# Performance work log

Measured on AMD Instinct MI355X. Metric: run time of the kernel, lower is better.

The kernel has to match this reference:

```python
import jax, jax.numpy as jnp
import numpy as np
import math

D = 512  # feature dim (must equal Lv for the final bmm)

def setup_inputs() -> dict:
    key = jax.random.key(0)
    k1, k2, k3 = jax.random.split(key, 3)
    B, Lp, Lq, Lv = 32, 1024, 1024, 512
    linear_pre = jax.random.normal(k1, (B, Lp, D), dtype=jnp.float32)
    linear_q = jax.random.normal(k2, (B, Lq, D), dtype=jnp.float32)
    linear_v = jax.random.normal(k3, (B, Lv, D), dtype=jnp.float32)
    return {"linear_pre": linear_pre, "linear_q": linear_q, "linear_v": linear_v}

def reference(linear_pre, linear_q, linear_v):
    scale = 1.0 / math.sqrt(D)
    # Two parallel softmax-attention streams (exp / sum == softmax over last dim).
    # attnp: [B, Lp, Lq], attne: [B, Lq, Lv]
    attnp = jax.nn.softmax(jnp.einsum('bpd,bqd->bpq', linear_pre, linear_q) * scale, axis=-1)
    attne = jax.nn.softmax(jnp.einsum('bqd,bvd->bqv', linear_q, linear_v) * scale, axis=-1)
    # dropout is identity in eval mode (deterministic reference)
    precompute = jnp.einsum('bpq,bqd->bpd', attnp, linear_q)   # [B, Lp, D]
    energy = jnp.einsum('bqv,bvd->bqd', attne, linear_v)       # [B, Lq, D]
    # final bmm requires D == Lv
    weightedContext = jnp.einsum('bqv,bvd->bqd', energy, linear_v)  # [B, Lq, D]
    return (weightedContext, energy, precompute)
```

## Files before the change

kernel.cpp:

```cpp
#include <hip/hip_runtime.h>

#define BATCH 32
#define LP 1024
#define LQ 1024
#define LV 512
#define DIM 512

typedef __bf16 bf16x8 __attribute__((ext_vector_type(8)));
typedef float f32x4 __attribute__((ext_vector_type(4)));
typedef unsigned short ushort_t;
typedef unsigned short us8 __attribute__((ext_vector_type(8)));

__device__ __forceinline__ ushort_t f2bf(float f) {
  unsigned int u = __float_as_uint(f);
  unsigned int r = (u + 0x7FFFu + ((u >> 16) & 1u)) >> 16;
  return (ushort_t)r;
}

__device__ __forceinline__ void async16(const void* g, void* l) {
  __builtin_amdgcn_global_load_lds(
      (const __attribute__((address_space(1))) unsigned int*)g,
      (__attribute__((address_space(3))) unsigned int*)l, 16, 0, 0);
}

__global__ __launch_bounds__(256)
void cvt_kernel(const float* __restrict__ in, ushort_t* __restrict__ out) {
  int i = blockIdx.x * blockDim.x + threadIdx.x;
  const float4* p = (const float4*)in;
  float4 a = p[i * 2], b = p[i * 2 + 1];
  us8 h;
  h[0] = f2bf(a.x); h[1] = f2bf(a.y); h[2] = f2bf(a.z); h[3] = f2bf(a.w);
  h[4] = f2bf(b.x); h[5] = f2bf(b.y); h[6] = f2bf(b.z); h[7] = f2bf(b.w);
  *(us8*)&out[(size_t)i * 8] = h;
}

__global__ void transpose_cvt(const float* __restrict__ in, ushort_t* __restrict__ outT,
                              ushort_t* __restrict__ outR, int R, int C) {
  __shared__ ushort_t tile[32][33];
  int b = blockIdx.z;
  int c0 = blockIdx.x * 32, r0 = blockIdx.y * 32;
  const float* inb = in + (size_t)b * R * C;
  ushort_t* outTb = outT + (size_t)b * R * C;
  ushort_t* outRb = outR + (size_t)b * R * C;
  int x = threadIdx.x, y = threadIdx.y;
#pragma unroll
  for (int k = 0; k < 4; ++k) {
    int r = r0 + y + k * 8;
    ushort_t h = f2bf(inb[(size_t)r * C + c0 + x]);
    tile[y + k * 8][x] = h;
    outRb[(size_t)r * C + c0 + x] = h;
  }
  __syncthreads();
#pragma unroll
  for (int k = 0; k < 4; ++k) {
    int c = c0 + y + k * 8;
    outTb[(size_t)c * R + r0 + x] = tile[x][y + k * 8];
  }
}

__global__ __launch_bounds__(256)
void score_bf16_kernel(const ushort_t* __restrict__ A, const ushort_t* __restrict__ BT,
                       ushort_t* __restrict__ P, float* __restrict__ lsum,
                       int M, int N, int K) {
  __shared__ ushort_t sA[128 * 32];
  __shared__ ushort_t sB[128 * 32];
  int b = blockIdx.z;
  int m0 = blockIdx.x * 128, n0 = blockIdx.y * 128;
  const ushort_t* Ab = A + ((size_t)b * M + m0) * K;
  const ushort_t* Bb = BT + ((size_t)b * N + n0) * K;
  int tid = threadIdx.x;
  int lane = tid & 63, w = tid >> 6;
  int wm = w >> 1, wn = w & 1;
  int quad = lane >> 4, low = lane & 15;

  f32x4 acc[4][4];
  f32x4 zero = {0.f, 0.f, 0.f, 0.f};
#pragma unroll
  for (int i = 0; i < 4; ++i)
#pragma unroll
    for (int j = 0; j < 4; ++j) acc[i][j] = zero;

  for (int kt = 0; kt < K; kt += 32) {
#pragma unroll
    for (int j = 0; j < 2; ++j) {
      int cb = w * 128 + j * 64;
      int c = cb + lane;
      int r = c >> 2, kc = c & 3;
      async16(Ab + (size_t)r * K + kt + kc * 8, &sA[cb * 8]);
      async16(Bb + (size_t)r * K + kt + kc * 8, &sB[cb * 8]);
    }
    __syncthreads();
    bf16x8 af[4], bfr[4];
#pragma unroll
    for (int t = 0; t < 4; ++t) {
      af[t]  = *(const bf16x8*)&sA[(wm * 64 + t * 16 + low) * 32 + quad * 8];
      bfr[t] = *(const bf16x8*)&sB[(wn * 64 + t * 16 + low) * 32 + quad * 8];
    }
#pragma unroll
    for (int i = 0; i < 4; ++i)
#pragma unroll
      for (int j = 0; j < 4; ++j)
        acc[i][j] = __builtin_amdgcn_mfma_f32_16x16x32_bf16(af[i], bfr[j], acc[i][j], 0, 0, 0);
    __syncthreads();
  }

  const float sc = 0.04419417382415922f;
  size_t pb = (size_t)b * M * N;
#pragma unroll
  for (int i = 0; i < 4; ++i) {
    int gr0 = m0 + wm * 64 + i * 16 + quad * 4;
#pragma unroll
    for (int r = 0; r < 4; ++r) {
      int gr = gr0 + r;
      float rs = 0.f;
#pragma unroll
      for (int j = 0; j < 4; ++j) {
        float p = __expf(acc[i][j][r] * sc);
        rs += p;
        int gc = n0 + wn * 64 + j * 16 + low;
        P[pb + (size_t)gr * N + gc] = f2bf(p);
      }
      rs += __shfl_xor(rs, 1);
      rs += __shfl_xor(rs, 2);
      rs += __shfl_xor(rs, 4);
      rs += __shfl_xor(rs, 8);
      if (low == 0) atomicAdd(&lsum[(size_t)b * M + gr], rs);
    }
  }
}

template <bool DIV, bool OUT2>
__global__ __launch_bounds__(256)
void gemm_bt_kernel(const ushort_t* __restrict__ A, const ushort_t* __restrict__ BT,
                    const float* __restrict__ lsum, float* __restrict__ out,
                    ushort_t* __restrict__ out2, int M, int N, int K) {
  __shared__ ushort_t sA[128 * 32];
  __shared__ ushort_t sB[128 * 32];
  int b = blockIdx.z;
  int m0 = blockIdx.x * 128, n0 = blockIdx.y * 128;
  const ushort_t* Ab = A + ((size_t)b * M + m0) * K;
  const ushort_t* Bb = BT + ((size_t)b * N + n0) * K;
  int tid = threadIdx.x;
  int lane = tid & 63, w = tid >> 6;
  int wm = w >> 1, wn = w & 1;
  int quad = lane >> 4, low = lane & 15;

  f32x4 acc[4][4];
  f32x4 zero = {0.f, 0.f, 0.f, 0.f};
#pragma unroll
  for (int i = 0; i < 4; ++i)
#pragma unroll
    for (int j = 0; j < 4; ++j) acc[i][j] = zero;

  for (int kt = 0; kt < K; kt += 32) {
#pragma unroll
    for (int j = 0; j < 2; ++j) {
      int cb = w * 128 + j * 64;
      int c = cb + lane;
      int r = c >> 2, kc = c & 3;
      async16(Ab + (size_t)r * K + kt + kc * 8, &sA[cb * 8]);
      async16(Bb + (size_t)r * K + kt + kc * 8, &sB[cb * 8]);
    }
    __syncthreads();
    bf16x8 af[4], bfr[4];
#pragma unroll
    for (int t = 0; t < 4; ++t) {
      af[t]  = *(const bf16x8*)&sA[(wm * 64 + t * 16 + low) * 32 + quad * 8];
      bfr[t] = *(const bf16x8*)&sB[(wn * 64 + t * 16 + low) * 32 + quad * 8];
    }
#pragma unroll
    for (int i = 0; i < 4; ++i)
#pragma unroll
      for (int j = 0; j < 4; ++j)
        acc[i][j] = __builtin_amdgcn_mfma_f32_16x16x32_bf16(af[i], bfr[j], acc[i][j], 0, 0, 0);
    __syncthreads();
  }

  size_t ob = (size_t)b * M * N;
#pragma unroll
  for (int i = 0; i < 4; ++i) {
    int gr0 = m0 + wm * 64 + i * 16 + quad * 4;
#pragma unroll
    for (int r = 0; r < 4; ++r) {
      int gr = gr0 + r;
      float inv = 1.f;
      if (DIV) inv = 1.f / lsum[(size_t)b * M + gr];
#pragma unroll
      for (int j = 0; j < 4; ++j) {
        int gc = n0 + wn * 64 + j * 16 + low;
        float o = acc[i][j][r] * inv;
        out[ob + (size_t)gr * N + gc] = o;
        if (OUT2) out2[ob + (size_t)gr * N + gc] = f2bf(o);
      }
    }
  }
}

extern "C" void kernel_launch(void* const* d_in, const int* in_sizes, int n_in,
                              void* d_out, int out_size, void* d_ws, size_t ws_size,
                              hipStream_t stream) {
  (void)in_sizes; (void)n_in; (void)out_size; (void)ws_size;
  const float* pre = (const float*)d_in[0];
  const float* q   = (const float*)d_in[1];
  const float* v   = (const float*)d_in[2];

  float* out      = (float*)d_out;
  float* wc       = out;
  float* energy   = out + (size_t)BATCH * LQ * DIM;
  float* precomp  = out + 2 * (size_t)BATCH * LQ * DIM;

  char* ws = (char*)d_ws;
  size_t off = 0;
  auto alloc = [&](size_t bytes) {
    void* p = ws + off;
    off += (bytes + 255) & ~(size_t)255;
    return p;
  };
  ushort_t* preB = (ushort_t*)alloc((size_t)BATCH * LP * DIM * 2);
  ushort_t* qB   = (ushort_t*)alloc((size_t)BATCH * LQ * DIM * 2);
  ushort_t* vB   = (ushort_t*)alloc((size_t)BATCH * LV * DIM * 2);
  ushort_t* qT   = (ushort_t*)alloc((size_t)BATCH * DIM * LQ * 2);
  ushort_t* vT   = (ushort_t*)alloc((size_t)BATCH * DIM * LV * 2);
  ushort_t* Pp   = (ushort_t*)alloc((size_t)BATCH * LP * LQ * 2);
  ushort_t* Pe   = (ushort_t*)alloc((size_t)BATCH * LQ * LV * 2);
  ushort_t* Ebf  = (ushort_t*)alloc((size_t)BATCH * LQ * DIM * 2);
  float* lp = (float*)alloc((size_t)BATCH * LP * 4);
  float* le = (float*)alloc((size_t)BATCH * LQ * 4);

  hipMemsetAsync(lp, 0, (size_t)BATCH * (LP + LQ) * 4, stream);

  cvt_kernel<<<(size_t)BATCH * LP * DIM / 8 / 256, 256, 0, stream>>>(pre, preB);
  transpose_cvt<<<dim3(DIM / 32, LQ / 32, BATCH), dim3(32, 8), 0, stream>>>(q, qT, qB, LQ, DIM);
  transpose_cvt<<<dim3(DIM / 32, LV / 32, BATCH), dim3(32, 8), 0, stream>>>(v, vT, vB, LV, DIM);

  score_bf16_kernel<<<dim3(LP / 128, LQ / 128, BATCH), 256, 0, stream>>>(
      preB, qB, Pp, lp, LP, LQ, DIM);
  score_bf16_kernel<<<dim3(LQ / 128, LV / 128, BATCH), 256, 0, stream>>>(
      qB, vB, Pe, le, LQ, LV, DIM);

  gemm_bt_kernel<true, false><<<dim3(LP / 128, DIM / 128, BATCH), 256, 0, stream>>>(
      Pp, qT, lp, precomp, nullptr, LP, DIM, LQ);
  gemm_bt_kernel<true, true><<<dim3(LQ / 128, DIM / 128, BATCH), 256, 0, stream>>>(
      Pe, vT, le, energy, Ebf, LQ, DIM, LV);
  gemm_bt_kernel<false, false><<<dim3(LQ / 128, DIM / 128, BATCH), 256, 0, stream>>>(
      Ebf, vT, nullptr, wc, nullptr, LQ, DIM, LV);
}
```

Measured before the change: 598.8 us.

## Replace GEMMs with 256x256-tile double-buffered pipelined MFMA kernel

Merges the score and output GEMM kernels into one templated 256x256-tile kernel with 512 threads and 128KB of dynamic LDS. It double-buffers K tiles of 64 with async global-to-LDS loads, explicit vmcnt waits and raw barriers, XOR-swizzles the LDS columns to avoid bank conflicts, and raises wave priority around the MFMA blocks. The goal is more data reuse per tile and hiding global load latency behind matrix math. The cost is higher register and LDS pressure, fewer blocks (4x fewer tiles, e.g. 256 for the Pe score GEMM), and fragile hand-written synchronisation.

```diff
diff --git a/kernel.cpp b/kernel.cpp
--- a/kernel.cpp
+++ b/kernel.cpp
@@ -22,6 +22,9 @@
       (const __attribute__((address_space(1))) unsigned int*)g,
       (__attribute__((address_space(3))) unsigned int*)l, 16, 0, 0);
 }
+
+#define BARRIER() asm volatile("s_barrier" ::: "memory")
+#define VMCNT(n) asm volatile("s_waitcnt vmcnt(" #n ")" ::: "memory")
 
 __global__ __launch_bounds__(256)
 void cvt_kernel(const float* __restrict__ in, ushort_t* __restrict__ out) {
@@ -58,143 +61,163 @@
   }
 }
 
-__global__ __launch_bounds__(256)
-void score_bf16_kernel(const ushort_t* __restrict__ A, const ushort_t* __restrict__ BT,
-                       ushort_t* __restrict__ P, float* __restrict__ lsum,
-                       int M, int N, int K) {
-  __shared__ ushort_t sA[128 * 32];
-  __shared__ ushort_t sB[128 * 32];
+template <int H>
+__device__ __forceinline__ void mm8(f32x4 (&acc)[8][4], const bf16x8 (&af)[4],
+                                    const bf16x8 (&bfv)[4]) {
+  __builtin_amdgcn_s_setprio(1);
+#pragma unroll
+  for (int i = 0; i < 4; ++i)
+#pragma unroll
+    for (int j = 0; j < 4; ++j)
+      acc[H * 4 + i][j] =
+          __builtin_amdgcn_mfma_f32_16x16x32_bf16(af[i], bfv[j], acc[H * 4 + i][j], 0, 0, 0);
+  __builtin_amdgcn_s_setprio(0);
+}
+
+template <int MODE, bool OUT2>
+__global__ __launch_bounds__(512, 2)
+void gemm256(const ushort_t* __restrict__ A, const ushort_t* __restrict__ BT,
+             const float* __restrict__ lsumIn, float* __restrict__ outF,
+             ushort_t* __restrict__ outB, float* __restrict__ lsumOut,
+             int M, int N, int K) {
+  extern __shared__ ushort_t smem[];
+  ushort_t* sA = smem;
+  ushort_t* sB = smem + 32768;
+
   int b = blockIdx.z;
-  int m0 = blockIdx.x * 128, n0 = blockIdx.y * 128;
+  int m0 = blockIdx.x * 256, n0 = blockIdx.y * 256;
   const ushort_t* Ab = A + ((size_t)b * M + m0) * K;
   const ushort_t* Bb = BT + ((size_t)b * N + n0) * K;
   int tid = threadIdx.x;
-  int lane = tid & 63, w = tid >> 6;
-  int wm = w >> 1, wn = w & 1;
-  int quad = lane >> 4, low = lane & 15;
-
-  f32x4 acc[4][4];
+  int l = tid & 63, w = tid >> 6;
+  int wm = w >> 2, wn = w & 3;
+  int low = l & 15, quad = l >> 4;
+  const int colsw = (quad * 8) ^ ((l & 8) ? 16 : 0);
+
+  int NT = K >> 6;
+
+  f32x4 acc[8][4];
   f32x4 zero = {0.f, 0.f, 0.f, 0.f};
 #pragma unroll
-  for (int i = 0; i < 4; ++i)
+  for (int i = 0; i < 8; ++i)
 #pragma unroll
     for (int j = 0; j < 4; ++j) acc[i][j] = zero;
 
-  for (int kt = 0; kt < K; kt += 32) {
-#pragma unroll
-    for (int j = 0; j < 2; ++j) {
-      int cb = w * 128 + j * 64;
-      int c = cb + lane;
-      int r = c >> 2, kc = c & 3;
-      async16(Ab + (size_t)r * K + kt + kc * 8, &sA[cb * 8]);
-      async16(Bb + (size_t)r * K + kt + kc * 8, &sB[cb * 8]);
-    }
-    __syncthreads();
-    bf16x8 af[4], bfr[4];
-#pragma unroll
-    for (int t = 0; t < 4; ++t) {
-      af[t]  = *(const bf16x8*)&sA[(wm * 64 + t * 16 + low) * 32 + quad * 8];
-      bfr[t] = *(const bf16x8*)&sB[(wn * 64 + t * 16 + low) * 32 + quad * 8];
-    }
-#pragma unroll
-    for (int i = 0; i < 4; ++i)
-#pragma unroll
-      for (int j = 0; j < 4; ++j)
-        acc[i][j] = __builtin_amdgcn_mfma_f32_16x16x32_bf16(af[i], bfr[j], acc[i][j], 0, 0, 0);
-    __syncthreads();
-  }
-
-  const float sc = 0.04419417382415922f;
-  size_t pb = (size_t)b * M * N;
-#pragma unroll
-  for (int i = 0; i < 4; ++i) {
-    int gr0 = m0 + wm * 64 + i * 16 + quad * 4;
-#pragma unroll
-    for (int r = 0; r < 4; ++r) {
-      int gr = gr0 + r;
-      float rs = 0.f;
-#pragma unroll
-      for (int j = 0; j < 4; ++j) {
-        float p = __expf(acc[i][j][r] * sc);
-        rs += p;
-        int gc = n0 + wn * 64 + j * 16 + low;
-        P[pb + (size_t)gr * N + gc] = f2bf(p);
+  auto stageT = [&](const ushort_t* gb, ushort_t* sbase, int T, int kh) {
+    ushort_t* hb = sbase + (((T & 1) << 1) + kh) * 8192;
+    int kc0 = (T << 6) + (kh << 5);
+#pragma unroll
+    for (int ii = 0; ii < 2; ++ii) {
+      int o = w * 128 + ii * 64;
+      int ol = o + l;
+      int cc = ((ol & 3) ^ ((l >> 4) & 2)) << 3;
+      async16(gb + (size_t)(ol >> 2) * K + kc0 + cc, hb + o * 8);
+    }
+  };
+  auto ldA = [&](bf16x8 (&af)[4], int buf, int k, int h) {
+    const ushort_t* base = sA + ((buf << 1) + k) * 8192 + colsw;
+    int r0 = wm * 128 + h * 64 + low;
+#pragma unroll
+    for (int i = 0; i < 4; ++i) af[i] = *(const bf16x8*)&base[(r0 + i * 16) * 32];
+  };
+  auto ldB = [&](bf16x8 (&bfv)[4], int buf, int k) {
+    const ushort_t* base = sB + ((buf << 1) + k) * 8192 + colsw;
+    int r0 = wn * 64 + low;
+#pragma unroll
+    for (int j = 0; j < 4; ++j) bfv[j] = *(const bf16x8*)&base[(r0 + j * 16) * 32];
+  };
+
+  stageT(Ab, sA, 0, 0);
+  stageT(Bb, sB, 0, 0);
+  stageT(Ab, sA, 0, 1);
+  stageT(Bb, sB, 0, 1);
+  VMCNT(4);
+  if (NT > 1) {
+    stageT(Bb, sB, 1, 0);
+    stageT(Ab, sA, 1, 0);
+    stageT(Bb, sB, 1, 1);
+    VMCNT(6);
+  } else {
+    VMCNT(0);
+  }
+  BARRIER();
+
+  bf16x8 af[4], bfv[4];
+  for (int T = 0; T < NT; ++T) {
+    int buf = T & 1;
+    ldB(bfv, buf, 0);
+    ldA(af, buf, 0, 0);
+    if (T + 1 < NT) stageT(Ab, sA, T + 1, 1);
+    BARRIER();
+    mm8<0>(acc, af, bfv);
+    BARRIER();
+    ldA(af, buf, 0, 1);
+    if (T + 2 < NT) stageT(Bb, sB, T + 2, 0);
+    BARRIER();
+    mm8<1>(acc, af, bfv);
+    BARRIER();
+    ldB(bfv, buf, 1);
+    ldA(af, buf, 1, 0);
+    if (T + 2 < NT) stageT(Ab, sA, T + 2, 0);
+    BARRIER();
+    mm8<0>(acc, af, bfv);
+    BARRIER();
+    ldA(af, buf, 1, 1);
+    if (T + 2 < NT) stageT(Bb, sB, T + 2, 1);
+    if (T + 1 < NT) {
+      if (T + 2 < NT) { VMCNT(6); } else { VMCNT(0); }
+    }
+    BARRIER();
+    mm8<1>(acc, af, bfv);
+    BARRIER();
+  }
+
+  size_t ob = (size_t)b * M * N;
+  if (MODE == 2) {
+    const float sc = 0.04419417382415922f;
+#pragma unroll
+    for (int i = 0; i < 8; ++i) {
+      int gr0 = m0 + wm * 128 + i * 16 + quad * 4;
+#pragma unroll
+      for (int r = 0; r < 4; ++r) {
+        int gr = gr0 + r;
+        float rs = 0.f;
+#pragma unroll
+        for (int j = 0; j < 4; ++j) {
+          float p = __expf(acc[i][j][r] * sc);
+          rs += p;
+          int gc = n0 + wn * 64 + j * 16 + low;
+          outB[ob + (size_t)gr * N + gc] = f2bf(p);
+        }
+        rs += __shfl_xor(rs, 1);
+        rs += __shfl_xor(rs, 2);
+        rs += __shfl_xor(rs, 4);
+        rs += __shfl_xor(rs, 8);
+        if (low == 0) atomicAdd(&lsumOut[(size_t)b * M + gr], rs);
       }
-      rs += __shfl_xor(rs, 1);
-      rs += __shfl_xor(rs, 2);
-      rs += __shfl_xor(rs, 4);
-      rs += __shfl_xor(rs, 8);
-      if (low == 0) atomicAdd(&lsum[(size_t)b * M + gr], rs);
-    }
-  }
-}
-
-template <bool DIV, bool OUT2>
-__global__ __launch_bounds__(256)
-void gemm_bt_kernel(const ushort_t* __restrict__ A, const ushort_t* __restrict__ BT,
-                    const float* __restrict__ lsum, float* __restrict__ out,
-                    ushort_t* __restrict__ out2, int M, int N, int K) {
-  __shared__ ushort_t sA[128 * 32];
-  __shared__ ushort_t sB[128 * 32];
-  int b = blockIdx.z;
-  int m0 = blockIdx.x * 128, n0 = blockIdx.y * 128;
-  const ushort_t* Ab = A + ((size_t)b * M + m0) * K;
-  const ushort_t* Bb = BT + ((size_t)b * N + n0) * K;
-  int tid = threadIdx.x;
-  int lane = tid & 63, w = tid >> 6;
-  int wm = w >> 1, wn = w & 1;
-  int quad = lane >> 4, low = lane & 15;
-
-  f32x4 acc[4][4];
-  f32x4 zero = {0.f, 0.f, 0.f, 0.f};
-#pragma unroll
-  for (int i = 0; i < 4; ++i)
-#pragma unroll
-    for (int j = 0; j < 4; ++j) acc[i][j] = zero;
-
-  for (int kt = 0; kt < K; kt += 32) {
-#pragma unroll
-    for (int j = 0; j < 2; ++j) {
-      int cb = w * 128 + j * 64;
-      int c = cb + lane;
-      int r = c >> 2, kc = c & 3;
-      async16(Ab + (size_t)r * K + kt + kc * 8, &sA[cb * 8]);
-      async16(Bb + (size_t)r * K + kt + kc * 8, &sB[cb * 8]);
-    }
-    __syncthreads();
-    bf16x8 af[4], bfr[4];
-#pragma unroll
-    for (int t = 0; t < 4; ++t) {
-      af[t]  = *(const bf16x8*)&sA[(wm * 64 + t * 16 + low) * 32 + quad * 8];
-      bfr[t] = *(const bf16x8*)&sB[(wn * 64 + t * 16 + low) * 32 + quad * 8];
-    }
-#pragma unroll
-    for (int i = 0; i < 4; ++i)
-#pragma unroll
-      for (int j = 0; j < 4; ++j)
-        acc[i][j] = __builtin_amdgcn_mfma_f32_16x16x32_bf16(af[i], bfr[j], acc[i][j], 0, 0, 0);
-    __syncthreads();
-  }
-
-  size_t ob = (size_t)b * M * N;
-#pragma unroll
-  for (int i = 0; i < 4; ++i) {
-    int gr0 = m0 + wm * 64 + i * 16 + quad * 4;
-#pragma unroll
-    for (int r = 0; r < 4; ++r) {
-      int gr = gr0 + r;
-      float inv = 1.f;
-      if (DIV) inv = 1.f / lsum[(size_t)b * M + gr];
-#pragma unroll
-      for (int j = 0; j < 4; ++j) {
-        int gc = n0 + wn * 64 + j * 16 + low;
-        float o = acc[i][j][r] * inv;
-        out[ob + (size_t)gr * N + gc] = o;
-        if (OUT2) out2[ob + (size_t)gr * N + gc] = f2bf(o);
+    }
+  } else {
+#pragma unroll
+    for (int i = 0; i < 8; ++i) {
+      int gr0 = m0 + wm * 128 + i * 16 + quad * 4;
+#pragma unroll
+      for (int r = 0; r < 4; ++r) {
+        int gr = gr0 + r;
+        float inv = 1.f;
+        if (MODE == 1) inv = 1.f / lsumIn[(size_t)b * M + gr];
+#pragma unroll
+        for (int j = 0; j < 4; ++j) {
+          int gc = n0 + wn * 64 + j * 16 + low;
+          float o = acc[i][j][r] * inv;
+          outF[ob + (size_t)gr * N + gc] = o;
+          if (OUT2) outB[ob + (size_t)gr * N + gc] = f2bf(o);
+        }
       }
     }
   }
 }
+
+#define LDS_BYTES 131072
 
 extern "C" void kernel_launch(void* const* d_in, const int* in_sizes, int n_in,
                               void* d_out, int out_size, void* d_ws, size_t ws_size,
@@ -227,21 +250,34 @@
   float* lp = (float*)alloc((size_t)BATCH * LP * 4);
   float* le = (float*)alloc((size_t)BATCH * LQ * 4);
 
+  static bool attr_done = false;
+  if (!attr_done) {
+    attr_done = true;
+    hipFuncSetAttribute(reinterpret_cast<const void*>(&gemm256<2, false>),
+                        hipFuncAttributeMaxDynamicSharedMemorySize, LDS_BYTES);
+    hipFuncSetAttribute(reinterpret_cast<const void*>(&gemm256<1, false>),
+                        hipFuncAttributeMaxDynamicSharedMemorySize, LDS_BYTES);
+    hipFuncSetAttribute(reinterpret_cast<const void*>(&gemm256<1, true>),
+                        hipFuncAttributeMaxDynamicSharedMemorySize, LDS_BYTES);
+    hipFuncSetAttribute(reinterpret_cast<const void*>(&gemm256<0, false>),
+                        hipFuncAttributeMaxDynamicSharedMemorySize, LDS_BYTES);
+  }
+
   hipMemsetAsync(lp, 0, (size_t)BATCH * (LP + LQ) * 4, stream);
 
   cvt_kernel<<<(size_t)BATCH * LP * DIM / 8 / 256, 256, 0, stream>>>(pre, preB);
   transpose_cvt<<<dim3(DIM / 32, LQ / 32, BATCH), dim3(32, 8), 0, stream>>>(q, qT, qB, LQ, DIM);
   transpose_cvt<<<dim3(DIM / 32, LV / 32, BATCH), dim3(32, 8), 0, stream>>>(v, vT, vB, LV, DIM);
 
-  score_bf16_kernel<<<dim3(LP / 128, LQ / 128, BATCH), 256, 0, stream>>>(
-      preB, qB, Pp, lp, LP, LQ, DIM);
-  score_bf16_kernel<<<dim3(LQ / 128, LV / 128, BATCH), 256, 0, stream>>>(
-      qB, vB, Pe, le, LQ, LV, DIM);
-
-  gemm_bt_kernel<true, false><<<dim3(LP / 128, DIM / 128, BATCH), 256, 0, stream>>>(
-      Pp, qT, lp, precomp, nullptr, LP, DIM, LQ);
-  gemm_bt_kernel<true, true><<<dim3(LQ / 128, DIM / 128, BATCH), 256, 0, stream>>>(
-      Pe, vT, le, energy, Ebf, LQ, DIM, LV);
-  gemm_bt_kernel<false, false><<<dim3(LQ / 128, DIM / 128, BATCH), 256, 0, stream>>>(
-      Ebf, vT, nullptr, wc, nullptr, LQ, DIM, LV);
-}
+  gemm256<2, false><<<dim3(LP / 256, LQ / 256, BATCH), 512, LDS_BYTES, stream>>>(
+      preB, qB, nullptr, nullptr, Pp, lp, LP, LQ, DIM);
+  gemm256<2, false><<<dim3(LQ / 256, LV / 256, BATCH), 512, LDS_BYTES, stream>>>(
+      qB, vB, nullptr, nullptr, Pe, le, LQ, LV, DIM);
+
+  gemm256<1, false><<<dim3(LP / 256, DIM / 256, BATCH), 512, LDS_BYTES, stream>>>(
+      Pp, qT, lp, precomp, nullptr, nullptr, LP, DIM, LQ);
+  gemm256<1, true><<<dim3(LQ / 256, DIM / 256, BATCH), 512, LDS_BYTES, stream>>>(
+      Pe, vT, le, energy, Ebf, nullptr, LQ, DIM, LV);
+  gemm256<0, false><<<dim3(LQ / 256, DIM / 256, BATCH), 512, LDS_BYTES, stream>>>(
+      Ebf, vT, nullptr, wc, nullptr, nullptr, LQ, DIM, LV);
+}
```

Result: faster. 530.8 us (-11.4%).
